# Kernel optimization log

Measured on AMD Instinct MI355X. Metric: run time of the kernel, lower is better.

The kernel has to match this reference:

```python
import jax, jax.numpy as jnp
import numpy as np

D_EMBED = 1024
N_HEAD = 16
MAX_SEQ = 512
D_K = D_EMBED // N_HEAD


def setup_inputs() -> dict:
    key = jax.random.key(0)
    ks = jax.random.split(key, 10)
    B, S, D = 16, MAX_SEQ, D_EMBED
    std = 1.0 / np.sqrt(D)
    x = jax.random.normal(ks[0], (B, S, D), dtype=jnp.float32)
    Wq = jax.random.normal(ks[1], (D, D), dtype=jnp.float32) * std
    bq = jnp.zeros((D,), dtype=jnp.float32)
    Wk = jax.random.normal(ks[2], (D, D), dtype=jnp.float32) * std
    bk = jnp.zeros((D,), dtype=jnp.float32)
    Wv = jax.random.normal(ks[3], (D, D), dtype=jnp.float32) * std
    bv = jnp.zeros((D,), dtype=jnp.float32)
    Wo = jax.random.normal(ks[4], (D, D), dtype=jnp.float32) * std
    bo = jnp.zeros((D,), dtype=jnp.float32)
    rel_table = jax.random.normal(ks[5], (2 * MAX_SEQ - 1, N_HEAD), dtype=jnp.float32) * 0.02
    return {"x": x, "Wq": Wq, "bq": bq, "Wk": Wk, "bk": bk,
            "Wv": Wv, "bv": bv, "Wo": Wo, "bo": bo, "rel_table": rel_table}


def reference(x, Wq, bq, Wk, bk, Wv, bv, Wo, bo, rel_table):
    B, S, D = x.shape
    H, dk = N_HEAD, D_K
    scale = 1.0 / np.sqrt(dk)
    # QKV projections -> (B, H, S, dk)
    q = (x @ Wq.T + bq).reshape(B, S, H, dk).transpose(0, 2, 1, 3)
    k = (x @ Wk.T + bk).reshape(B, S, H, dk).transpose(0, 2, 1, 3)
    v = (x @ Wv.T + bv).reshape(B, S, H, dk).transpose(0, 2, 1, 3)
    # raw scores (B, H, S, S)
    scores = jnp.einsum('bhsd,bhtd->bhst', q * scale, k)
    # relative position bias: index[i,j] = i + (S-1-j), table (2S-1, H)
    i = jnp.arange(S)
    idx = i[:, None] + (S - 1 - i)[None, :]          # (S, S)
    bias = rel_table[idx]                             # (S, S, H)
    scores = scores + bias.transpose(2, 0, 1)[None]   # (1, H, S, S)
    probs = jax.nn.softmax(scores, axis=-1)
    attn = jnp.einsum('bhst,bhtd->bhsd', probs, v)
    attn = attn.transpose(0, 2, 1, 3).reshape(B, S, D)
    return attn @ Wo.T + bo
```

## Files before the change

kernel.cpp:

```cpp
#include <hip/hip_runtime.h>
#include <cstdint>
#include <cstddef>

typedef unsigned short u16;
typedef __attribute__((ext_vector_type(8))) short bf16x8;
typedef __attribute__((ext_vector_type(4))) float f32x4;

__device__ __forceinline__ u16 f2bf(float f) {
  unsigned u = __builtin_bit_cast(unsigned, f);
  return (u16)((u + 0x7FFFu + ((u >> 16) & 1u)) >> 16);
}

__device__ __forceinline__ void gload_lds16(const void* g, void* l) {
  __builtin_amdgcn_global_load_lds(
      (const __attribute__((address_space(1))) void*)g,
      (__attribute__((address_space(3))) void*)l,
      16, 0, 0);
}

__global__ void cast_all_kernel(const float* __restrict__ x,
                                const float* __restrict__ wq, const float* __restrict__ wk,
                                const float* __restrict__ wv, const float* __restrict__ wo,
                                u16* __restrict__ ox,
                                u16* __restrict__ oq, u16* __restrict__ ok,
                                u16* __restrict__ ov, u16* __restrict__ oo) {
  const int which = blockIdx.y;
  const float* in = which == 0 ? x  : which == 1 ? wq : which == 2 ? wk
                                    : which == 3 ? wv : wo;
  u16* out        = which == 0 ? ox : which == 1 ? oq : which == 2 ? ok
                                    : which == 3 ? ov : oo;
  const int n4 = which == 0 ? 8192 * 1024 / 4 : 262144;
  int i = blockIdx.x * blockDim.x + threadIdx.x;
  int stride = gridDim.x * blockDim.x;
  for (int idx = i; idx < n4; idx += stride) {
    float4 f = ((const float4*)in)[idx];
    ushort4 o = make_ushort4(f2bf(f.x), f2bf(f.y), f2bf(f.z), f2bf(f.w));
    ((ushort4*)out)[idx] = o;
  }
}

__global__ __launch_bounds__(256, 2)
void gemm_qkv(const u16* __restrict__ A, const u16* __restrict__ W,
              const float* __restrict__ bq, const float* __restrict__ bk,
              const float* __restrict__ bvv,
              u16* __restrict__ qout, u16* __restrict__ kout, u16* __restrict__ vt) {
  __shared__ u16 Alds[128 * 32];
  __shared__ u16 Blds[128 * 32];
  const int tid  = threadIdx.x;
  const int lane = tid & 63;
  const int wid  = tid >> 6;
  const int orig = blockIdx.x;
  const int swz  = (orig & 7) * 192 + (orig >> 3);
  const int m0 = (swz / 24) * 128;
  const int n0 = (swz % 24) * 128;
  const int wm = (wid >> 1) * 64;
  const int wn = (wid & 1) * 64;

  f32x4 acc[4][4] = {};

  const int srow = tid >> 2;
  const int scol = (tid & 3) * 8;
  const u16* Ag = A + (size_t)(m0 + srow) * 1024 + scol;
  const u16* Wg = W + (size_t)(n0 + srow) * 1024 + scol;
  u16* Al = &Alds[wid * 16 * 32];
  u16* Bl = &Blds[wid * 16 * 32];

  for (int k0 = 0; k0 < 1024; k0 += 32) {
    __syncthreads();
    gload_lds16(Ag + k0,             Al);
    gload_lds16(Ag + 64 * 1024 + k0, Al + 64 * 32);
    gload_lds16(Wg + k0,             Bl);
    gload_lds16(Wg + 64 * 1024 + k0, Bl + 64 * 32);
    __syncthreads();
    bf16x8 a[4], bb[4];
#pragma unroll
    for (int i = 0; i < 4; ++i)
      a[i] = *(const bf16x8*)&Alds[(wm + i * 16 + (lane & 15)) * 32 + (lane >> 4) * 8];
#pragma unroll
    for (int i = 0; i < 4; ++i)
      bb[i] = *(const bf16x8*)&Blds[(wn + i * 16 + (lane & 15)) * 32 + (lane >> 4) * 8];
#pragma unroll
    for (int mi = 0; mi < 4; ++mi)
#pragma unroll
      for (int ni = 0; ni < 4; ++ni)
        acc[mi][ni] = __builtin_amdgcn_mfma_f32_16x16x32_bf16(a[mi], bb[ni], acc[mi][ni], 0, 0, 0);
  }

  const int region = n0 >> 10;
#pragma unroll
  for (int ni = 0; ni < 4; ++ni) {
    const int n  = n0 + wn + ni * 16 + (lane & 15);
    const int nn = n & 1023;
    const float bias = region == 0 ? bq[nn] : region == 1 ? bk[nn] : bvv[nn];
#pragma unroll
    for (int mi = 0; mi < 4; ++mi) {
      const int mBase = m0 + wm + mi * 16 + ((lane >> 4) << 2);
      if (region == 0) {
#pragma unroll
        for (int r = 0; r < 4; ++r)
          qout[(size_t)(mBase + r) * 1024 + nn] = f2bf(acc[mi][ni][r] + bias);
      } else if (region == 1) {
#pragma unroll
        for (int r = 0; r < 4; ++r)
          kout[(size_t)(mBase + r) * 1024 + nn] = f2bf(acc[mi][ni][r] + bias);
      } else {
        const int batch = mBase >> 9;
        const int s = mBase & 511;
        const int h = nn >> 6;
        const int d = nn & 63;
        ushort4 ov = make_ushort4(f2bf(acc[mi][ni][0] + bias), f2bf(acc[mi][ni][1] + bias),
                                  f2bf(acc[mi][ni][2] + bias), f2bf(acc[mi][ni][3] + bias));
        *(ushort4*)&vt[((size_t)((batch * 16 + h) * 64 + d) << 9) + s] = ov;
      }
    }
  }
}

__global__ __launch_bounds__(256, 2)
void gemm_out(const u16* __restrict__ A, const u16* __restrict__ W,
              const float* __restrict__ bias, float* __restrict__ outp) {
  __shared__ u16 Alds[128 * 32];
  __shared__ u16 Blds[128 * 32];
  const int tid  = threadIdx.x;
  const int lane = tid & 63;
  const int wid  = tid >> 6;
  const int orig = blockIdx.x;
  const int swz  = (orig & 7) * 64 + (orig >> 3);
  const int m0 = (swz >> 3) * 128;
  const int n0 = (swz & 7) * 128;
  const int wm = (wid >> 1) * 64;
  const int wn = (wid & 1) * 64;

  f32x4 acc[4][4] = {};

  const int srow = tid >> 2;
  const int scol = (tid & 3) * 8;
  const u16* Ag = A + (size_t)(m0 + srow) * 1024 + scol;
  const u16* Wg = W + (size_t)(n0 + srow) * 1024 + scol;
  u16* Al = &Alds[wid * 16 * 32];
  u16* Bl = &Blds[wid * 16 * 32];

  for (int k0 = 0; k0 < 1024; k0 += 32) {
    __syncthreads();
    gload_lds16(Ag + k0,             Al);
    gload_lds16(Ag + 64 * 1024 + k0, Al + 64 * 32);
    gload_lds16(Wg + k0,             Bl);
    gload_lds16(Wg + 64 * 1024 + k0, Bl + 64 * 32);
    __syncthreads();
    bf16x8 a[4], bb[4];
#pragma unroll
    for (int i = 0; i < 4; ++i)
      a[i] = *(const bf16x8*)&Alds[(wm + i * 16 + (lane & 15)) * 32 + (lane >> 4) * 8];
#pragma unroll
    for (int i = 0; i < 4; ++i)
      bb[i] = *(const bf16x8*)&Blds[(wn + i * 16 + (lane & 15)) * 32 + (lane >> 4) * 8];
#pragma unroll
    for (int mi = 0; mi < 4; ++mi)
#pragma unroll
      for (int ni = 0; ni < 4; ++ni)
        acc[mi][ni] = __builtin_amdgcn_mfma_f32_16x16x32_bf16(a[mi], bb[ni], acc[mi][ni], 0, 0, 0);
  }

#pragma unroll
  for (int ni = 0; ni < 4; ++ni) {
    const int n = n0 + wn + ni * 16 + (lane & 15);
    const float bv = bias[n];
#pragma unroll
    for (int mi = 0; mi < 4; ++mi) {
      const int mBase = m0 + wm + mi * 16 + ((lane >> 4) << 2);
#pragma unroll
      for (int r = 0; r < 4; ++r)
        outp[(size_t)(mBase + r) * 1024 + n] = acc[mi][ni][r] + bv;
    }
  }
}

__global__ __launch_bounds__(256, 3)
void attn_kernel(const u16* __restrict__ Q, const u16* __restrict__ K,
                 const u16* __restrict__ Vt, const float* __restrict__ rel,
                 u16* __restrict__ Oa) {
  __shared__ u16 Kl[128 * 64];
  __shared__ u16 Vl[64 * 128];
  __shared__ u16 Pl[4][16 * 136];
  __shared__ float tcol[576];

  const int tid  = threadIdx.x;
  const int lane = tid & 63;
  const int wid  = tid >> 6;
  const int g    = lane >> 4;
  const int lc   = lane & 15;

  const int orig = blockIdx.x;
  const int swz  = (orig & 7) * 256 + (orig >> 3);
  const int qb    = swz & 7;
  const int bh    = swz >> 3;
  const int h     = bh & 15;
  const int batch = bh >> 4;
  const int q0    = qb * 64;

  const size_t xbase  = (size_t)batch * 512 * 1024 + (size_t)h * 64;
  const size_t vtbase = (size_t)(batch * 16 + h) * 64 * 512;

  for (int u = tid; u < 575; u += 256)
    tcol[u] = rel[(size_t)(q0 + u) * 16 + h];

#define STAGE_TILE(t)                                                              \
  {                                                                                \
    _Pragma("unroll")                                                              \
    for (int j = 0; j < 4; ++j) {                                                  \
      const int kr = j * 32 + (tid >> 3);                                          \
      const int sk = (tid & 7) ^ (kr & 7);                                         \
      gload_lds16(K + xbase + (size_t)((t) * 128 + kr) * 1024 + sk * 8,            \
                  &Kl[j * 2048 + wid * 512]);                                      \
      const int vr = j * 16 + (tid >> 4);                                          \
      const int sv = (tid & 15) ^ (vr & 7);                                        \
      gload_lds16(Vt + vtbase + (size_t)vr * 512 + (t) * 128 + sv * 8,             \
                  &Vl[j * 2048 + wid * 512]);                                      \
    }                                                                              \
  }

  STAGE_TILE(0)

  bf16x8 aq[2];
#pragma unroll
  for (int ks = 0; ks < 2; ++ks)
    aq[ks] = *(const bf16x8*)&Q[xbase + (size_t)(q0 + wid * 16 + lc) * 1024 + ks * 32 + g * 8];

  float m_run[4], l_run[4];
  f32x4 acc_o[4] = {};
#pragma unroll
  for (int r = 0; r < 4; ++r) { m_run[r] = -1e30f; l_run[r] = 0.f; }

  __syncthreads();

  const float scale = 0.125f;
  for (int t = 0; t < 4; ++t) {
    f32x4 acc[8] = {};
#pragma unroll
    for (int f = 0; f < 8; ++f) {
      const int rl = f * 16 + lc;
#pragma unroll
      for (int ks = 0; ks < 2; ++ks) {
        bf16x8 bk = *(const bf16x8*)&Kl[rl * 64 + (((ks * 4 + g) ^ (rl & 7)) * 8)];
        acc[f] = __builtin_amdgcn_mfma_f32_16x16x32_bf16(aq[ks], bk, acc[f], 0, 0, 0);
      }
    }
    const int ubase = wid * 16 + 4 * g + 511 - t * 128 - lc;
#pragma unroll
    for (int f = 0; f < 8; ++f)
#pragma unroll
      for (int r = 0; r < 4; ++r)
        acc[f][r] = acc[f][r] * scale + tcol[ubase + r - f * 16];

    float tm[4];
#pragma unroll
    for (int r = 0; r < 4; ++r) {
      float m = fmaxf(fmaxf(fmaxf(acc[0][r], acc[1][r]), fmaxf(acc[2][r], acc[3][r])),
                      fmaxf(fmaxf(acc[4][r], acc[5][r]), fmaxf(acc[6][r], acc[7][r])));
      m = fmaxf(m, __shfl_xor(m, 1));
      m = fmaxf(m, __shfl_xor(m, 2));
      m = fmaxf(m, __shfl_xor(m, 4));
      m = fmaxf(m, __shfl_xor(m, 8));
      tm[r] = m;
    }
    float al[4];
#pragma unroll
    for (int r = 0; r < 4; ++r) {
      const float mn = fmaxf(m_run[r], tm[r]);
      al[r] = __expf(m_run[r] - mn);
      m_run[r] = mn;
    }
    float ts[4] = {};
#pragma unroll
    for (int f = 0; f < 8; ++f)
#pragma unroll
      for (int r = 0; r < 4; ++r) {
        const float e = __expf(acc[f][r] - m_run[r]);
        ts[r] += e;
        Pl[wid][(4 * g + r) * 136 + f * 16 + lc] = f2bf(e);
      }
#pragma unroll
    for (int r = 0; r < 4; ++r) {
      float s = ts[r];
      s += __shfl_xor(s, 1);
      s += __shfl_xor(s, 2);
      s += __shfl_xor(s, 4);
      s += __shfl_xor(s, 8);
      l_run[r] = l_run[r] * al[r] + s;
    }
#pragma unroll
    for (int dblk = 0; dblk < 4; ++dblk)
#pragma unroll
      for (int r = 0; r < 4; ++r)
        acc_o[dblk][r] *= al[r];

#pragma unroll
    for (int ks = 0; ks < 4; ++ks) {
      bf16x8 ap = *(const bf16x8*)&Pl[wid][lc * 136 + ks * 32 + g * 8];
#pragma unroll
      for (int dblk = 0; dblk < 4; ++dblk) {
        const int dr = dblk * 16 + lc;
        bf16x8 bv = *(const bf16x8*)&Vl[dr * 128 + (((ks * 4 + g) ^ (dr & 7)) * 8)];
        acc_o[dblk] = __builtin_amdgcn_mfma_f32_16x16x32_bf16(ap, bv, acc_o[dblk], 0, 0, 0);
      }
    }

    if (t < 3) {
      __syncthreads();
      STAGE_TILE(t + 1)
      __syncthreads();
    }
  }
#undef STAGE_TILE

#pragma unroll
  for (int dblk = 0; dblk < 4; ++dblk)
#pragma unroll
    for (int r = 0; r < 4; ++r) {
      const int row = q0 + wid * 16 + 4 * g + r;
      Oa[((size_t)batch * 512 + row) * 1024 + h * 64 + dblk * 16 + lc] =
          f2bf(acc_o[dblk][r] / l_run[r]);
    }
}

extern "C" void kernel_launch(void* const* d_in, const int* in_sizes, int n_in,
                              void* d_out, int out_size, void* d_ws, size_t ws_size,
                              hipStream_t stream) {
  (void)in_sizes; (void)n_in; (void)out_size; (void)ws_size;
  const float* x   = (const float*)d_in[0];
  const float* Wq  = (const float*)d_in[1];
  const float* bq  = (const float*)d_in[2];
  const float* Wk  = (const float*)d_in[3];
  const float* bk  = (const float*)d_in[4];
  const float* Wv  = (const float*)d_in[5];
  const float* bv  = (const float*)d_in[6];
  const float* Wo  = (const float*)d_in[7];
  const float* bo  = (const float*)d_in[8];
  const float* rel = (const float*)d_in[9];
  float* out = (float*)d_out;

  u16* p = (u16*)d_ws;
  u16* xbf = p;  p += (size_t)8192 * 1024;
  u16* wqb = p;  p += (size_t)1024 * 1024;
  u16* wkb = p;  p += (size_t)1024 * 1024;
  u16* wvb = p;  p += (size_t)1024 * 1024;
  u16* wob = p;  p += (size_t)1024 * 1024;
  u16* qbf = p;  p += (size_t)8192 * 1024;
  u16* kbf = p;  p += (size_t)8192 * 1024;
  u16* vtb = p;  p += (size_t)8192 * 1024;
  u16* abf = p;  p += (size_t)8192 * 1024;

  cast_all_kernel<<<dim3(1024, 5), 256, 0, stream>>>(x, Wq, Wk, Wv, Wo,
                                                     xbf, wqb, wkb, wvb, wob);

  gemm_qkv<<<1536, 256, 0, stream>>>(xbf, wqb, bq, bk, bv, qbf, kbf, vtb);

  attn_kernel<<<2048, 256, 0, stream>>>(qbf, kbf, vtb, rel, abf);

  gemm_out<<<512, 256, 0, stream>>>(abf, wob, bo, out);
}
```

Baseline: 248.4 us.

## Rewrite QKV GEMM as 256x256 tile, 8-wave, double-buffered pipelined kernel

Replaces the 128x128, 4-wave QKV projection GEMM with a 256x256 tile, 512-thread kernel that uses K-step 64, XOR-swizzled LDS layout and double buffering. Global-to-LDS loads for the next K tile are interleaved with MFMA quarters under fine-grained barriers and s_setprio. The aim is to hide global load latency, raise arithmetic intensity per LDS byte and avoid LDS bank conflicts. It uses 128KB of LDS and many accumulator registers, so it depends on occupancy, and the hand-written schedule is complex.

```diff
diff --git a/kernel.cpp b/kernel.cpp
--- a/kernel.cpp
+++ b/kernel.cpp
@@ -39,62 +39,124 @@
   }
 }
 
-__global__ __launch_bounds__(256, 2)
-void gemm_qkv(const u16* __restrict__ A, const u16* __restrict__ W,
-              const float* __restrict__ bq, const float* __restrict__ bk,
-              const float* __restrict__ bvv,
-              u16* __restrict__ qout, u16* __restrict__ kout, u16* __restrict__ vt) {
-  __shared__ u16 Alds[128 * 32];
-  __shared__ u16 Blds[128 * 32];
+
+#define STAGE_A8(BUF, H, T)                                                    \
+  { const u16* s_ = Asrc + (size_t)(H) * 131072 + (T) * 64;                    \
+    u16* d_ = &lds[(BUF) * 32768 + (H) * 8192 + wid * 512];                    \
+    gload_lds16(s_, d_);                                                       \
+    gload_lds16(s_ + 65536, d_ + 4096); }
+
+#define STAGE_B8(BUF, H, T)                                                    \
+  { const u16* s_ = Wsrc + (size_t)(H) * 131072 + (T) * 64;                    \
+    u16* d_ = &lds[(BUF) * 32768 + 16384 + (H) * 8192 + wid * 512];            \
+    gload_lds16(s_, d_);                                                       \
+    gload_lds16(s_ + 65536, d_ + 4096); }
+
+#define LOAD_A8(BUF, MH)                                                       \
+  _Pragma("unroll") for (int j_ = 0; j_ < 4; ++j_) {                           \
+    const int r_ = ((MH) * 4 + j_) * 16 + lc;                                  \
+    const int o_ = (BUF) * 32768 + abase + r_ * 64;                            \
+    a[j_][0] = *(const bf16x8*)&lds[o_ + ((g ^ (r_ & 7)) * 8)];                \
+    a[j_][1] = *(const bf16x8*)&lds[o_ + (((4 + g) ^ (r_ & 7)) * 8)];          \
+  }
+
+#define LOAD_B8(BUF, NH, BREG)                                                 \
+  _Pragma("unroll") for (int j_ = 0; j_ < 2; ++j_) {                           \
+    const int r_ = brlo + ((NH) * 2 + j_) * 16 + lc;                           \
+    const int o_ = (BUF) * 32768 + bbase + r_ * 64;                            \
+    BREG[j_][0] = *(const bf16x8*)&lds[o_ + ((g ^ (r_ & 7)) * 8)];             \
+    BREG[j_][1] = *(const bf16x8*)&lds[o_ + (((4 + g) ^ (r_ & 7)) * 8)];       \
+  }
+
+#define MMAQ8(MH, NH, BREG)                                                    \
+  __builtin_amdgcn_s_setprio(1);                                               \
+  _Pragma("unroll") for (int j_ = 0; j_ < 4; ++j_)                             \
+    _Pragma("unroll") for (int n_ = 0; n_ < 2; ++n_) {                         \
+      acc[(MH) * 4 + j_][(NH) * 2 + n_] =                                      \
+          __builtin_amdgcn_mfma_f32_16x16x32_bf16(                             \
+              a[j_][0], BREG[n_][0], acc[(MH) * 4 + j_][(NH) * 2 + n_], 0, 0, 0); \
+      acc[(MH) * 4 + j_][(NH) * 2 + n_] =                                      \
+          __builtin_amdgcn_mfma_f32_16x16x32_bf16(                             \
+              a[j_][1], BREG[n_][1], acc[(MH) * 4 + j_][(NH) * 2 + n_], 0, 0, 0); \
+    }                                                                          \
+  __builtin_amdgcn_s_setprio(0);
+
+#define BAR1a                                                                  \
+  __builtin_amdgcn_s_barrier();                                                \
+  asm volatile("s_waitcnt lgkmcnt(0)" ::: "memory");                           \
+  __builtin_amdgcn_sched_barrier(0);
+
+#define BAR2a __builtin_amdgcn_s_barrier();
+
+#define VMW(N) asm volatile("s_waitcnt vmcnt(" #N ")" ::: "memory");
+
+__global__ __launch_bounds__(512, 2)
+void gemm_qkv8(const u16* __restrict__ A, const u16* __restrict__ W,
+               const float* __restrict__ bq, const float* __restrict__ bk,
+               const float* __restrict__ bvv,
+               u16* __restrict__ qout, u16* __restrict__ kout, u16* __restrict__ vt) {
+  __shared__ u16 lds[65536];
   const int tid  = threadIdx.x;
   const int lane = tid & 63;
   const int wid  = tid >> 6;
+  const int wr   = wid >> 2;
+  const int wc   = wid & 3;
+  const int lc   = lane & 15;
+  const int g    = lane >> 4;
+
   const int orig = blockIdx.x;
-  const int swz  = (orig & 7) * 192 + (orig >> 3);
-  const int m0 = (swz / 24) * 128;
-  const int n0 = (swz % 24) * 128;
-  const int wm = (wid >> 1) * 64;
-  const int wn = (wid & 1) * 64;
-
-  f32x4 acc[4][4] = {};
-
-  const int srow = tid >> 2;
-  const int scol = (tid & 3) * 8;
-  const u16* Ag = A + (size_t)(m0 + srow) * 1024 + scol;
-  const u16* Wg = W + (size_t)(n0 + srow) * 1024 + scol;
-  u16* Al = &Alds[wid * 16 * 32];
-  u16* Bl = &Blds[wid * 16 * 32];
-
-  for (int k0 = 0; k0 < 1024; k0 += 32) {
-    __syncthreads();
-    gload_lds16(Ag + k0,             Al);
-    gload_lds16(Ag + 64 * 1024 + k0, Al + 64 * 32);
-    gload_lds16(Wg + k0,             Bl);
-    gload_lds16(Wg + 64 * 1024 + k0, Bl + 64 * 32);
-    __syncthreads();
-    bf16x8 a[4], bb[4];
-#pragma unroll
-    for (int i = 0; i < 4; ++i)
-      a[i] = *(const bf16x8*)&Alds[(wm + i * 16 + (lane & 15)) * 32 + (lane >> 4) * 8];
-#pragma unroll
-    for (int i = 0; i < 4; ++i)
-      bb[i] = *(const bf16x8*)&Blds[(wn + i * 16 + (lane & 15)) * 32 + (lane >> 4) * 8];
-#pragma unroll
-    for (int mi = 0; mi < 4; ++mi)
-#pragma unroll
-      for (int ni = 0; ni < 4; ++ni)
-        acc[mi][ni] = __builtin_amdgcn_mfma_f32_16x16x32_bf16(a[mi], bb[ni], acc[mi][ni], 0, 0, 0);
-  }
+  const int swz  = (orig & 7) * 48 + (orig >> 3);
+  const int m0 = (swz / 12) * 256;
+  const int n0 = (swz % 12) * 256;
+
+  const int srow  = tid >> 3;
+  const int scol8 = ((tid & 7) ^ (srow & 7)) * 8;
+  const u16* Asrc = A + (size_t)(m0 + srow) * 1024 + scol8;
+  const u16* Wsrc = W + (size_t)(n0 + srow) * 1024 + scol8;
+
+  const int abase = wr * 8192;
+  const int bbase = 16384 + (wc >> 1) * 8192;
+  const int brlo  = (wc & 1) * 64;
+
+  f32x4 acc[8][4] = {};
+  bf16x8 a[4][2], bA[2][2], bB[2][2];
+
+  STAGE_B8(0, 0, 0) STAGE_B8(0, 1, 0) STAGE_A8(0, 0, 0) STAGE_A8(0, 1, 0)
+  STAGE_B8(1, 0, 1) STAGE_B8(1, 1, 1)
+  VMW(4)
+  __builtin_amdgcn_s_barrier();
+
+  for (int i = 0; i < 7; ++i) {
+    const int tb  = 2 * i + 1;
+    const int ta2 = 2 * i + 2;
+    const int tb2 = 2 * i + 3;
+    LOAD_A8(0, 0) LOAD_B8(0, 0, bA) STAGE_A8(1, 0, tb) BAR1a MMAQ8(0, 0, bA) BAR2a
+    LOAD_B8(0, 1, bB) STAGE_A8(1, 1, tb) BAR1a MMAQ8(0, 1, bB) BAR2a
+    LOAD_A8(0, 1) STAGE_B8(0, 0, ta2) BAR1a MMAQ8(1, 0, bA) BAR2a
+    STAGE_B8(0, 1, ta2) BAR1a MMAQ8(1, 1, bB) VMW(4) BAR2a
+    LOAD_A8(1, 0) LOAD_B8(1, 0, bA) STAGE_A8(0, 0, ta2) BAR1a MMAQ8(0, 0, bA) BAR2a
+    LOAD_B8(1, 1, bB) STAGE_A8(0, 1, ta2) BAR1a MMAQ8(0, 1, bB) BAR2a
+    LOAD_A8(1, 1) STAGE_B8(1, 0, tb2) BAR1a MMAQ8(1, 0, bA) BAR2a
+    STAGE_B8(1, 1, tb2) BAR1a MMAQ8(1, 1, bB) VMW(4) BAR2a
+  }
+  LOAD_A8(0, 0) LOAD_B8(0, 0, bA) STAGE_A8(1, 0, 15) BAR1a MMAQ8(0, 0, bA) BAR2a
+  LOAD_B8(0, 1, bB) STAGE_A8(1, 1, 15) BAR1a MMAQ8(0, 1, bB) BAR2a
+  LOAD_A8(0, 1) BAR1a MMAQ8(1, 0, bA) BAR2a
+  BAR1a MMAQ8(1, 1, bB) VMW(0) BAR2a
+  LOAD_A8(1, 0) LOAD_B8(1, 0, bA) BAR1a MMAQ8(0, 0, bA) BAR2a
+  LOAD_B8(1, 1, bB) BAR1a MMAQ8(0, 1, bB) BAR2a
+  LOAD_A8(1, 1) BAR1a MMAQ8(1, 0, bA) BAR2a
+  BAR1a MMAQ8(1, 1, bB)
 
   const int region = n0 >> 10;
 #pragma unroll
   for (int ni = 0; ni < 4; ++ni) {
-    const int n  = n0 + wn + ni * 16 + (lane & 15);
-    const int nn = n & 1023;
+    const int col = n0 + wc * 64 + ni * 16 + lc;
+    const int nn = col & 1023;
     const float bias = region == 0 ? bq[nn] : region == 1 ? bk[nn] : bvv[nn];
 #pragma unroll
-    for (int mi = 0; mi < 4; ++mi) {
-      const int mBase = m0 + wm + mi * 16 + ((lane >> 4) << 2);
+    for (int mi = 0; mi < 8; ++mi) {
+      const int mBase = m0 + wr * 128 + mi * 16 + g * 4;
       if (region == 0) {
 #pragma unroll
         for (int r = 0; r < 4; ++r)
@@ -353,7 +415,7 @@
   cast_all_kernel<<<dim3(1024, 5), 256, 0, stream>>>(x, Wq, Wk, Wv, Wo,
                                                      xbf, wqb, wkb, wvb, wob);
 
-  gemm_qkv<<<1536, 256, 0, stream>>>(xbf, wqb, bq, bk, bv, qbf, kbf, vtb);
+  gemm_qkv8<<<384, 512, 0, stream>>>(xbf, wqb, bq, bk, bv, qbf, kbf, vtb);
 
   attn_kernel<<<2048, 256, 0, stream>>>(qbf, kbf, vtb, rel, abf);
 
```

Result: no change. 249.0 us (+0.2%).
